# Optimization experiments

Measured on AMD Instinct MI355X. Metric: run time of the kernel, lower is better.

## Reference

```python
import jax, jax.numpy as jnp
import numpy as np

VOCAB, EMB, HID, B, T = 32000, 256, 256, 64, 2048


def setup_inputs() -> dict:
    key = jax.random.key(0)
    ks = jax.random.split(key, 6)
    s = 1.0 / np.sqrt(HID)
    return {
        "source": jax.random.randint(ks[0], (B, T), 0, VOCAB),
        "embedding": jax.random.normal(ks[1], (VOCAB, EMB), dtype=jnp.float32) * 0.02,
        "W_ih": jax.random.uniform(ks[2], (EMB, HID), jnp.float32, -s, s),
        "W_hh": jax.random.uniform(ks[3], (HID, HID), jnp.float32, -s, s),
        "b_ih": jax.random.uniform(ks[4], (HID,), jnp.float32, -s, s),
        "b_hh": jax.random.uniform(ks[5], (HID,), jnp.float32, -s, s),
    }


def reference(source, embedding, W_ih, W_hh, b_ih, b_hh):
    # embedding lookup: [B, T, EMB]
    embedded = embedding[source]
    # scan over time with carried hidden state (RNNCellManual: tanh cell)
    xs = jnp.swapaxes(embedded, 0, 1)  # [T, B, EMB]

    def step(h, x_t):
        h_new = jnp.tanh(x_t @ W_ih + b_ih + h @ W_hh + b_hh)
        return h_new, None

    h0 = jnp.zeros((source.shape[0], W_hh.shape[0]), dtype=embedding.dtype)
    h_T, _ = jax.lax.scan(step, h0, xs)
    return h_T  # final hidden state [B, HID]
```

## Files before the change

kernel.cpp:

```cpp
#include <hip/hip_runtime.h>

#define TT 2048
#define BB 64
#define HH 256

typedef _Float16 half2_t __attribute__((ext_vector_type(2)));
typedef _Float16 half8_t __attribute__((ext_vector_type(8)));
typedef float f32x4 __attribute__((ext_vector_type(4)));

static __device__ __forceinline__ float fdot2(half2_t a, half2_t b, float c) {
#if __has_builtin(__builtin_amdgcn_fdot2)
  return __builtin_amdgcn_fdot2(a, b, c, false);
#else
  return c + (float)a[0] * (float)b[0] + (float)a[1] * (float)b[1];
#endif
}

__global__ void prep_kernel(const float* __restrict__ Wih, const float* __restrict__ Whh,
                            _Float16* __restrict__ WihT, _Float16* __restrict__ WhhT) {
  const int n = blockIdx.x;
  const int k = threadIdx.x;
  WihT[n * HH + k] = (_Float16)Wih[k * HH + n];
  WhhT[n * HH + k] = (_Float16)Whh[k * HH + n];
}

__global__ __launch_bounds__(256, 2) void embed_gemm_kernel(
    const int* __restrict__ source, const float* __restrict__ emb,
    const _Float16* __restrict__ WihT, const float* __restrict__ b_ih,
    const float* __restrict__ b_hh, _Float16* __restrict__ U) {
  const int t = blockIdx.x;
  const int nbase = blockIdx.y * 64;
  __shared__ __align__(16) _Float16 Bs[64][280];

  const int tid = threadIdx.x;
  for (int c = tid; c < 64 * 32; c += 256) {
    const int n = c >> 5;
    const int ko = (c & 31) * 8;
    *(half8_t*)&Bs[n][ko] = *(const half8_t*)(WihT + (size_t)(nbase + n) * HH + ko);
  }
  __syncthreads();

  const int lane = tid & 63;
  const int wave = tid >> 6;
  const int row16 = lane & 15;
  const int quad = lane >> 4;
  const int b = wave * 16 + row16;
  const int src = source[b * TT + t];
  const float* arow = emb + (size_t)src * HH + quad * 8;

  f32x4 acc[4];
#pragma unroll
  for (int ct = 0; ct < 4; ++ct) acc[ct] = (f32x4){0.f, 0.f, 0.f, 0.f};

#pragma unroll
  for (int kt = 0; kt < 8; ++kt) {
    const float4 x0 = *(const float4*)(arow + kt * 32);
    const float4 x1 = *(const float4*)(arow + kt * 32 + 4);
    half8_t af;
    af[0] = (_Float16)x0.x; af[1] = (_Float16)x0.y;
    af[2] = (_Float16)x0.z; af[3] = (_Float16)x0.w;
    af[4] = (_Float16)x1.x; af[5] = (_Float16)x1.y;
    af[6] = (_Float16)x1.z; af[7] = (_Float16)x1.w;
#pragma unroll
    for (int ct = 0; ct < 4; ++ct) {
      const half8_t bf = *(const half8_t*)&Bs[ct * 16 + row16][quad * 8 + kt * 32];
      acc[ct] = __builtin_amdgcn_mfma_f32_16x16x32_f16(af, bf, acc[ct], 0, 0, 0);
    }
  }

#pragma unroll
  for (int ct = 0; ct < 4; ++ct) {
    const int nn = nbase + ct * 16 + row16;
    const float bias = b_ih[nn] + b_hh[nn];
#pragma unroll
    for (int r = 0; r < 4; ++r) {
      const int bb = wave * 16 + quad * 4 + r;
      U[((size_t)t * BB + bb) * HH + nn] = (_Float16)(acc[ct][r] + bias);
    }
  }
}

__global__ __launch_bounds__(256)
__attribute__((amdgpu_waves_per_eu(1, 1)))
void rnn_scan_kernel(
    const _Float16* __restrict__ U, const _Float16* __restrict__ WhhT,
    float* __restrict__ out) {
  const int b = blockIdx.x;
  const int tid = threadIdx.x;
  const int w = tid >> 6;
  const int l = tid & 63;

  __shared__ __align__(16) _Float16 hbuf[HH];
  __shared__ float pbuf[2][HH][5];

  half8_t wreg[4][8];
#pragma unroll
  for (int j = 0; j < 4; ++j) {
    const _Float16* wp = WhhT + (size_t)(64 * j + l) * HH + 64 * w;
#pragma unroll
    for (int r = 0; r < 8; ++r) wreg[j][r] = *(const half8_t*)(wp + 8 * r);
  }

  hbuf[tid] = (_Float16)0.f;

  const _Float16* Up = U + b * HH + tid;
  _Float16 uc[8], un[8];
#pragma unroll
  for (int s = 0; s < 8; ++s) uc[s] = Up[(size_t)s * (BB * HH)];

  float hn = 0.f;
  __syncthreads();

  for (int tc = 0; tc < TT; tc += 8) {
    const int tn = (tc + 8) & (TT - 1);
#pragma unroll
    for (int s = 0; s < 8; ++s) un[s] = Up[(size_t)(tn + s) * (BB * HH)];

#pragma unroll
    for (int s = 0; s < 8; ++s) {
      const _Float16* hrow = hbuf + 64 * w;
      half8_t hv[8];
#pragma unroll
      for (int r = 0; r < 8; ++r) hv[r] = *(const half8_t*)(hrow + 8 * r);

      float a0 = 0.f, a1 = 0.f, a2 = 0.f, a3 = 0.f;
#pragma unroll
      for (int r = 0; r < 8; ++r) {
#pragma unroll
        for (int i = 0; i < 4; ++i) {
          const half2_t hh = {hv[r][2 * i], hv[r][2 * i + 1]};
          const half2_t w0 = {wreg[0][r][2 * i], wreg[0][r][2 * i + 1]};
          const half2_t w1 = {wreg[1][r][2 * i], wreg[1][r][2 * i + 1]};
          const half2_t w2 = {wreg[2][r][2 * i], wreg[2][r][2 * i + 1]};
          const half2_t w3 = {wreg[3][r][2 * i], wreg[3][r][2 * i + 1]};
          a0 = fdot2(hh, w0, a0);
          a1 = fdot2(hh, w1, a1);
          a2 = fdot2(hh, w2, a2);
          a3 = fdot2(hh, w3, a3);
        }
      }

      pbuf[s & 1][l][w]       = a0;
      pbuf[s & 1][64 + l][w]  = a1;
      pbuf[s & 1][128 + l][w] = a2;
      pbuf[s & 1][192 + l][w] = a3;

      asm volatile("s_waitcnt lgkmcnt(0)\n\ts_barrier" ::: "memory");

      const float p0 = pbuf[s & 1][tid][0];
      const float p1 = pbuf[s & 1][tid][1];
      const float p2 = pbuf[s & 1][tid][2];
      const float p3 = pbuf[s & 1][tid][3];
      const float y = (p0 + p1) + (p2 + p3);
      const float a = (float)uc[s] + y;
      const float e = __builtin_amdgcn_exp2f(a * 2.885390081777927f);
      hn = 1.f - 2.f * __builtin_amdgcn_rcpf(e + 1.f);
      hbuf[tid] = (_Float16)hn;
    }
#pragma unroll
    for (int s = 0; s < 8; ++s) uc[s] = un[s];
  }
  out[(size_t)b * HH + tid] = hn;
}

extern "C" void kernel_launch(void* const* d_in, const int* in_sizes, int n_in,
                              void* d_out, int out_size, void* d_ws, size_t ws_size,
                              hipStream_t stream) {
  const int*   source = (const int*)d_in[0];
  const float* emb    = (const float*)d_in[1];
  const float* Wih    = (const float*)d_in[2];
  const float* Whh    = (const float*)d_in[3];
  const float* bih    = (const float*)d_in[4];
  const float* bhh    = (const float*)d_in[5];
  float* out = (float*)d_out;

  char* ws = (char*)d_ws;
  _Float16* U    = (_Float16*)ws;
  _Float16* WihT = (_Float16*)(ws + 67108864);
  _Float16* WhhT = (_Float16*)(ws + 67239936);

  prep_kernel<<<dim3(256), dim3(256), 0, stream>>>(Wih, Whh, WihT, WhhT);
  embed_gemm_kernel<<<dim3(TT, 4), dim3(256), 0, stream>>>(source, emb, WihT, bih, bhh, U);
  rnn_scan_kernel<<<dim3(BB), dim3(256), 0, stream>>>(U, WhhT, out);
}
```

Baseline: 1.086 ms.

## Restructure RNN scan to 512 threads with swizzle reduction and one barrier

The recurrent scan now runs 512 threads per batch row. Each group of 4 lanes owns two output columns and splits the K dimension into 4 chunks of 64. Partial sums are reduced across the 4 lanes with ds_swizzle instead of through a shared-memory partial buffer, and the hidden state is double-buffered so each timestep needs a single barrier instead of a write/barrier/read cycle. This cuts the per-step LDS traffic and the serial dot length on the critical path. In exchange it runs twice the waves per block and adds cross-lane swizzle latency.

```diff
diff --git a/kernel.cpp b/kernel.cpp
--- a/kernel.cpp
+++ b/kernel.cpp
@@ -14,6 +14,14 @@
 #else
   return c + (float)a[0] * (float)b[0] + (float)a[1] * (float)b[1];
 #endif
+}
+static __device__ __forceinline__ half2_t bch2(unsigned int u) {
+  return __builtin_bit_cast(half2_t, u);
+}
+template <int PAT>
+static __device__ __forceinline__ float swz_add(float x) {
+  const int yi = __builtin_amdgcn_ds_swizzle(__builtin_bit_cast(int, x), PAT);
+  return x + __builtin_bit_cast(float, yi);
 }
 
 __global__ void prep_kernel(const float* __restrict__ Wih, const float* __restrict__ Whh,
@@ -80,8 +88,8 @@
   }
 }
 
-__global__ __launch_bounds__(256)
-__attribute__((amdgpu_waves_per_eu(1, 1)))
+__global__ __launch_bounds__(512)
+__attribute__((amdgpu_waves_per_eu(2, 2)))
 void rnn_scan_kernel(
     const _Float16* __restrict__ U, const _Float16* __restrict__ WhhT,
     float* __restrict__ out) {
@@ -89,21 +97,44 @@
   const int tid = threadIdx.x;
   const int w = tid >> 6;
   const int l = tid & 63;
-
-  __shared__ __align__(16) _Float16 hbuf[HH];
-  __shared__ float pbuf[2][HH][5];
-
-  half8_t wreg[4][8];
-#pragma unroll
-  for (int j = 0; j < 4; ++j) {
-    const _Float16* wp = WhhT + (size_t)(64 * j + l) * HH + 64 * w;
-#pragma unroll
-    for (int r = 0; r < 8; ++r) wreg[j][r] = *(const half8_t*)(wp + 8 * r);
-  }
-
-  hbuf[tid] = (_Float16)0.f;
-
-  const _Float16* Up = U + b * HH + tid;
+  const int kp = l & 3;
+  const int ng = l >> 2;
+  const int n0 = 32 * w + 2 * ng;
+  const int nfin = n0 + (kp & 1);
+
+  __shared__ __align__(16) _Float16 hbuf[2][4][72];
+
+  half2_t w2[2][32];
+#pragma unroll
+  for (int j = 0; j < 2; ++j) {
+    const uint4* wp = (const uint4*)(WhhT + (size_t)(n0 + j) * HH + 64 * kp);
+#pragma unroll
+    for (int r = 0; r < 8; ++r) {
+      const uint4 q = wp[r];
+      w2[j][4 * r + 0] = bch2(q.x); w2[j][4 * r + 1] = bch2(q.y);
+      w2[j][4 * r + 2] = bch2(q.z); w2[j][4 * r + 3] = bch2(q.w);
+    }
+  }
+  asm volatile("" : "+v"(w2[0][0]), "+v"(w2[0][1]), "+v"(w2[0][2]), "+v"(w2[0][3]),
+                    "+v"(w2[0][4]), "+v"(w2[0][5]), "+v"(w2[0][6]), "+v"(w2[0][7]),
+                    "+v"(w2[0][8]), "+v"(w2[0][9]), "+v"(w2[0][10]), "+v"(w2[0][11]),
+                    "+v"(w2[0][12]), "+v"(w2[0][13]), "+v"(w2[0][14]), "+v"(w2[0][15]));
+  asm volatile("" : "+v"(w2[0][16]), "+v"(w2[0][17]), "+v"(w2[0][18]), "+v"(w2[0][19]),
+                    "+v"(w2[0][20]), "+v"(w2[0][21]), "+v"(w2[0][22]), "+v"(w2[0][23]),
+                    "+v"(w2[0][24]), "+v"(w2[0][25]), "+v"(w2[0][26]), "+v"(w2[0][27]),
+                    "+v"(w2[0][28]), "+v"(w2[0][29]), "+v"(w2[0][30]), "+v"(w2[0][31]));
+  asm volatile("" : "+v"(w2[1][0]), "+v"(w2[1][1]), "+v"(w2[1][2]), "+v"(w2[1][3]),
+                    "+v"(w2[1][4]), "+v"(w2[1][5]), "+v"(w2[1][6]), "+v"(w2[1][7]),
+                    "+v"(w2[1][8]), "+v"(w2[1][9]), "+v"(w2[1][10]), "+v"(w2[1][11]),
+                    "+v"(w2[1][12]), "+v"(w2[1][13]), "+v"(w2[1][14]), "+v"(w2[1][15]));
+  asm volatile("" : "+v"(w2[1][16]), "+v"(w2[1][17]), "+v"(w2[1][18]), "+v"(w2[1][19]),
+                    "+v"(w2[1][20]), "+v"(w2[1][21]), "+v"(w2[1][22]), "+v"(w2[1][23]),
+                    "+v"(w2[1][24]), "+v"(w2[1][25]), "+v"(w2[1][26]), "+v"(w2[1][27]),
+                    "+v"(w2[1][28]), "+v"(w2[1][29]), "+v"(w2[1][30]), "+v"(w2[1][31]));
+
+  for (int i = tid; i < 2 * 4 * 72; i += 512) ((_Float16*)hbuf)[i] = (_Float16)0.f;
+
+  const _Float16* Up = U + (size_t)b * HH + nfin;
   _Float16 uc[8], un[8];
 #pragma unroll
   for (int s = 0; s < 8; ++s) uc[s] = Up[(size_t)s * (BB * HH)];
@@ -118,49 +149,45 @@
 
 #pragma unroll
     for (int s = 0; s < 8; ++s) {
-      const _Float16* hrow = hbuf + 64 * w;
-      half8_t hv[8];
-#pragma unroll
-      for (int r = 0; r < 8; ++r) hv[r] = *(const half8_t*)(hrow + 8 * r);
-
-      float a0 = 0.f, a1 = 0.f, a2 = 0.f, a3 = 0.f;
+      const int t = tc + s;
+
+      const uint4* hp = (const uint4*)(&hbuf[t & 1][kp][0]);
+      half2_t h2[32];
 #pragma unroll
       for (int r = 0; r < 8; ++r) {
-#pragma unroll
-        for (int i = 0; i < 4; ++i) {
-          const half2_t hh = {hv[r][2 * i], hv[r][2 * i + 1]};
-          const half2_t w0 = {wreg[0][r][2 * i], wreg[0][r][2 * i + 1]};
-          const half2_t w1 = {wreg[1][r][2 * i], wreg[1][r][2 * i + 1]};
-          const half2_t w2 = {wreg[2][r][2 * i], wreg[2][r][2 * i + 1]};
-          const half2_t w3 = {wreg[3][r][2 * i], wreg[3][r][2 * i + 1]};
-          a0 = fdot2(hh, w0, a0);
-          a1 = fdot2(hh, w1, a1);
-          a2 = fdot2(hh, w2, a2);
-          a3 = fdot2(hh, w3, a3);
-        }
+        const uint4 q = hp[r];
+        h2[4 * r + 0] = bch2(q.x); h2[4 * r + 1] = bch2(q.y);
+        h2[4 * r + 2] = bch2(q.z); h2[4 * r + 3] = bch2(q.w);
       }
 
-      pbuf[s & 1][l][w]       = a0;
-      pbuf[s & 1][64 + l][w]  = a1;
-      pbuf[s & 1][128 + l][w] = a2;
-      pbuf[s & 1][192 + l][w] = a3;
-
-      asm volatile("s_waitcnt lgkmcnt(0)\n\ts_barrier" ::: "memory");
-
-      const float p0 = pbuf[s & 1][tid][0];
-      const float p1 = pbuf[s & 1][tid][1];
-      const float p2 = pbuf[s & 1][tid][2];
-      const float p3 = pbuf[s & 1][tid][3];
-      const float y = (p0 + p1) + (p2 + p3);
+      float a00 = 0.f, a01 = 0.f, a10 = 0.f, a11 = 0.f;
+#pragma unroll
+      for (int i = 0; i < 32; i += 2) {
+        a00 = fdot2(h2[i],     w2[0][i],     a00);
+        a10 = fdot2(h2[i],     w2[1][i],     a10);
+        a01 = fdot2(h2[i + 1], w2[0][i + 1], a01);
+        a11 = fdot2(h2[i + 1], w2[1][i + 1], a11);
+      }
+      float a0 = a00 + a01;
+      float a1 = a10 + a11;
+
+      a0 = swz_add<0x041F>(a0);
+      a1 = swz_add<0x041F>(a1);
+      a0 = swz_add<0x081F>(a0);
+      a1 = swz_add<0x081F>(a1);
+
+      const float y = (kp & 1) ? a1 : a0;
       const float a = (float)uc[s] + y;
       const float e = __builtin_amdgcn_exp2f(a * 2.885390081777927f);
       hn = 1.f - 2.f * __builtin_amdgcn_rcpf(e + 1.f);
-      hbuf[tid] = (_Float16)hn;
+      if (kp < 2) hbuf[(t + 1) & 1][nfin >> 6][nfin & 63] = (_Float16)hn;
+
+      asm volatile("s_waitcnt lgkmcnt(0)\n\ts_barrier" ::: "memory");
     }
 #pragma unroll
     for (int s = 0; s < 8; ++s) uc[s] = un[s];
   }
-  out[(size_t)b * HH + tid] = hn;
+  if (kp < 2) out[(size_t)b * HH + nfin] = hn;
 }
 
 extern "C" void kernel_launch(void* const* d_in, const int* in_sizes, int n_in,
@@ -181,5 +208,5 @@
 
   prep_kernel<<<dim3(256), dim3(256), 0, stream>>>(Wih, Whh, WihT, WhhT);
   embed_gemm_kernel<<<dim3(TT, 4), dim3(256), 0, stream>>>(source, emb, WihT, bih, bhh, U);
-  rnn_scan_kernel<<<dim3(BB), dim3(256), 0, stream>>>(U, WhhT, out);
-}
+  rnn_scan_kernel<<<dim3(BB), dim3(512), 0, stream>>>(U, WhhT, out);
+}
```

Result: slower. 1.230 ms (+13.2%).
